# Optimization experiments

Measured on AMD Instinct MI355X. Metric: run time of the kernel, lower is better.

The kernel has to match this reference:

```python
import jax, jax.numpy as jnp
import numpy as np
import math

B, C, F, W, NH = 2, 8, 1024, 512, 8
HD = F // NH


def conv2d(x, w, b):
    # NCHW 3x3 same-padding conv with bias
    y = jax.lax.conv_general_dilated(x, w, (1, 1), [(1, 1), (1, 1)],
                                     dimension_numbers=('NCHW', 'OIHW', 'NCHW'))
    return y + b[None, :, None, None]


def mc_linear(x, w):
    # per-channel linear over the feature (h) axis: (b,c,h,w) x (c,f,h) -> (b,c,f,w)
    return jnp.einsum('bchw,cfh->bcfw', x, w)


def split_heads(t):
    # (b,c,f,w) -> transpose(2,3) -> (b,c,w,f) -> (b,c,w,nh,hd) -> (b,c,nh,w,hd)
    b, c, f, w = t.shape
    return jnp.transpose(t.transpose(0, 1, 3, 2).reshape(b, c, w, NH, HD), (0, 1, 3, 2, 4))


def rotate_queries_or_keys(x):
    # lucidrains-style interleaved rotary over the sequence axis (dim -2)
    d, w = x.shape[-1], x.shape[-2]
    inv_freq = 1.0 / (10000.0 ** (jnp.arange(0, d, 2, dtype=jnp.float32) / d))
    freqs = jnp.arange(w, dtype=jnp.float32)[:, None] * inv_freq[None, :]  # (w, d/2)
    freqs = jnp.repeat(freqs, 2, axis=-1)  # (w, d)
    cos, sin = jnp.cos(freqs), jnp.sin(freqs)
    xp = x.reshape(*x.shape[:-1], d // 2, 2)
    x1, x2 = xp[..., 0], xp[..., 1]
    x_rot = jnp.stack((-x2, x1), axis=-1).reshape(x.shape)
    return x * cos + x_rot * sin


def _forward(x, prev_qk, wq_conv, bq_conv, wq_lin, wk_conv, bk_conv, wk_lin,
             wv_conv, bv_conv, wv_lin, wo_lin):
    b, c, h, w = x.shape
    q = rotate_queries_or_keys(split_heads(mc_linear(conv2d(x, wq_conv, bq_conv), wq_lin)))
    k = rotate_queries_or_keys(split_heads(mc_linear(conv2d(x, wk_conv, bk_conv), wk_lin)))
    v = split_heads(mc_linear(conv2d(x, wv_conv, bv_conv), wv_lin))
    # NOTE: original scales by sqrt(h) == sqrt(features), not sqrt(head_dim)
    qk = jnp.einsum('bcnqd,bcnkd->bcnqk', q, k) / math.sqrt(h) + prev_qk
    a = jnp.einsum('bcnqk,bcnkd->bcnqd', jax.nn.softmax(qk, axis=-1), v)
    a = jnp.transpose(a, (0, 1, 3, 2, 4)).reshape(b, c, w, h).transpose(0, 1, 3, 2)
    out = mc_linear(a, wo_lin)
    return out, qk


def setup_inputs() -> dict:
    key = jax.random.key(0)
    ks = jax.random.split(key, 10)
    s = 0.02
    return {
        'x': jax.random.normal(ks[0], (B, C, F, W), dtype=jnp.float32),
        'prev_qk': jax.random.normal(ks[1], (B, C, NH, W, W), dtype=jnp.float32) * 0.1,
        'wq_conv': jax.random.normal(ks[2], (C, C, 3, 3), dtype=jnp.float32) * s,
        'bq_conv': jnp.zeros((C,), dtype=jnp.float32),
        'wq_lin': jax.random.normal(ks[3], (C, F, F), dtype=jnp.float32) * s,
        'wk_conv': jax.random.normal(ks[4], (C, C, 3, 3), dtype=jnp.float32) * s,
        'bk_conv': jnp.zeros((C,), dtype=jnp.float32),
        'wk_lin': jax.random.normal(ks[5], (C, F, F), dtype=jnp.float32) * s,
        'wv_conv': jax.random.normal(ks[6], (C, C, 3, 3), dtype=jnp.float32) * s,
        'bv_conv': jnp.zeros((C,), dtype=jnp.float32),
        'wv_lin': jax.random.normal(ks[7], (C, F, F), dtype=jnp.float32) * s,
        'wo_lin': jax.random.normal(ks[8], (C, F, F), dtype=jnp.float32) * s,
    }


def reference(x, prev_qk, wq_conv, bq_conv, wq_lin, wk_conv, bk_conv, wk_lin,
              wv_conv, bv_conv, wv_lin, wo_lin):
    return _forward(x, prev_qk, wq_conv, bq_conv, wq_lin, wk_conv, bk_conv, wk_lin,
                    wv_conv, bv_conv, wv_lin, wo_lin)
```

## Files before the change

kernel.cpp:

```cpp
#include <hip/hip_runtime.h>
#include <stdint.h>


typedef float f32x4 __attribute__((ext_vector_type(4)));
typedef short s16x8 __attribute__((ext_vector_type(8)));

__device__ __forceinline__ short f2bf(float f) {
  union { float f; uint32_t u; } v; v.f = f;
  uint32_t r = v.u + 0x7FFFu + ((v.u >> 16) & 1u);
  return (short)(r >> 16);
}

__device__ __forceinline__ void g2l16(const void* g, void* l) {
  __builtin_amdgcn_global_load_lds(
      (const __attribute__((address_space(1))) void*)g,
      (__attribute__((address_space(3))) void*)l, 16, 0, 0);
}

__device__ __forceinline__ void gemm_core(const short* __restrict__ A,
                                          const short* __restrict__ B,
                                          int K, short* sA, short* sB,
                                          f32x4 (*acc)[4]) {
  const int tid = threadIdx.x;
  const int lane = tid & 63;
  const int wv = tid >> 6;
  const int wm = wv >> 1, wn = wv & 1;
  const int q = lane >> 4, cix = lane & 15;

  for (int k0 = 0; k0 < K; k0 += 32) {
    __syncthreads();
#pragma unroll
    for (int i = 0; i < 2; ++i) {
      int seg = wv + 4 * i;
      int m = seg * 16 + (lane >> 2);
      int ko = (lane & 3) * 8;
      g2l16(B + (size_t)m * K + k0 + ko, sB + seg * 512);
    }
#pragma unroll
    for (int i = 0; i < 2; ++i) {
      int seg = wv + 4 * i;
      int m = seg * 16 + (lane >> 2);
      int ko = (lane & 3) * 8;
      g2l16(A + (size_t)m * K + k0 + ko, sA + seg * 512);
    }
    __syncthreads();
    s16x8 afr[4], bfr[4];
#pragma unroll
    for (int i = 0; i < 4; ++i)
      afr[i] = *(const s16x8*)(sA + (wm * 64 + i * 16 + cix) * 32 + q * 8);
#pragma unroll
    for (int i = 0; i < 4; ++i)
      bfr[i] = *(const s16x8*)(sB + (wn * 64 + i * 16 + cix) * 32 + q * 8);
#pragma unroll
    for (int i = 0; i < 4; ++i)
#pragma unroll
      for (int j = 0; j < 4; ++j)
        acc[i][j] = __builtin_amdgcn_mfma_f32_16x16x32_bf16(afr[i], bfr[j],
                                                            acc[i][j], 0, 0, 0);
  }
}

__global__ void __launch_bounds__(256) k_cvt(
    const float* __restrict__ w0, const float* __restrict__ w1,
    const float* __restrict__ w2, const float* __restrict__ w3,
    short* __restrict__ Wb) {
  size_t i = (size_t)blockIdx.x * 256 + threadIdx.x;
#pragma unroll
  for (int r = 0; r < 4; ++r) {
    const float* s = (r == 0) ? w0 : (r == 1) ? w1 : (r == 2) ? w2 : w3;
    size_t v = i + (size_t)r * 2097152;
    float4 f = *(const float4*)(s + (i << 2));
    short4 o;
    o.x = f2bf(f.x); o.y = f2bf(f.y); o.z = f2bf(f.z); o.w = f2bf(f.w);
    *(short4*)(Wb + (v << 2)) = o;
  }
}

__global__ void __launch_bounds__(256) k_conv(
    const float* __restrict__ x,
    const float* __restrict__ wqc, const float* __restrict__ bqc,
    const float* __restrict__ wkc, const float* __restrict__ bkc,
    const float* __restrict__ wvc, const float* __restrict__ bvc,
    short* __restrict__ Yt) {
  __shared__ float xs[8][66][19];
  const int h0 = blockIdx.x * 64, w0 = blockIdx.y * 16, b = blockIdx.z;
  const int tid = threadIdx.x;
  for (int idx = tid; idx < 8 * 66 * 18; idx += 256) {
    int c = idx / (66 * 18);
    int rem = idx % (66 * 18);
    int r = rem / 18, cc = rem % 18;
    int h = h0 + r - 1, w = w0 + cc - 1;
    float v = 0.f;
    if (h >= 0 && h < 1024 && w >= 0 && w < 512)
      v = x[(((size_t)b * 8 + c) << 10 | (unsigned)h) * 512 + w];
    xs[c][r][cc] = v;
  }
  __syncthreads();
  const int hh = tid & 63;
  const int wv4 = tid >> 6;
  const size_t hgl = h0 + hh;
  for (int proj = 0; proj < 3; ++proj) {
    const float* wc = (proj == 0) ? wqc : ((proj == 1) ? wkc : wvc);
    const float* bc = (proj == 0) ? bqc : ((proj == 1) ? bkc : bvc);
    float a[4][8];
#pragma unroll
    for (int jj = 0; jj < 4; ++jj)
#pragma unroll
      for (int co = 0; co < 8; ++co) a[jj][co] = bc[co];
    for (int ci = 0; ci < 8; ++ci)
#pragma unroll
      for (int dh = 0; dh < 3; ++dh)
#pragma unroll
        for (int dw = 0; dw < 3; ++dw) {
          float xv[4];
#pragma unroll
          for (int jj = 0; jj < 4; ++jj)
            xv[jj] = xs[ci][hh + dh][wv4 * 4 + jj + dw];
          const int wi = ci * 9 + dh * 3 + dw;
#pragma unroll
          for (int co = 0; co < 8; ++co) {
            float wgt = wc[co * 72 + wi];
#pragma unroll
            for (int jj = 0; jj < 4; ++jj) a[jj][co] = fmaf(xv[jj], wgt, a[jj][co]);
          }
        }
#pragma unroll
    for (int jj = 0; jj < 4; ++jj) {
      size_t col = (size_t)b * 512 + w0 + wv4 * 4 + jj;
#pragma unroll
      for (int co = 0; co < 8; ++co)
        Yt[((size_t)(proj * 8 + co) << 20) + (col << 10) + hgl] = f2bf(a[jj][co]);
    }
  }
}

__global__ void __launch_bounds__(256) k_qkv(
    const short* __restrict__ Wb, const short* __restrict__ Yt,
    short* __restrict__ Qr, short* __restrict__ Kr, short* __restrict__ Vt) {
  __shared__ short sA[128 * 32], sB[128 * 32];
  const int L = blockIdx.x;
  const int lin = (L & 7) * 192 + (L >> 3);
  const int g = lin >> 6;
  const int t = lin & 63;
  const int proj = g >> 3, cq = g & 7;
  const int mt = t >> 3, nt = t & 7;
  const short* A = Wb + ((size_t)g << 20) + ((size_t)mt << 17);
  const short* B = Yt + ((size_t)g << 20) + ((size_t)nt << 17);
  const f32x4 fzero = {0.f, 0.f, 0.f, 0.f};
  f32x4 acc[4][4];
#pragma unroll
  for (int i = 0; i < 4; ++i)
#pragma unroll
    for (int j = 0; j < 4; ++j) acc[i][j] = fzero;
  gemm_core(A, B, 1024, sA, sB, acc);

  const int lane = threadIdx.x & 63, wv = threadIdx.x >> 6;
  const int wm = wv >> 1, wn = wv & 1, q = lane >> 4, cix = lane & 15;
  const int head = mt;
  if (proj == 2) {
#pragma unroll
    for (int mi = 0; mi < 4; ++mi) {
      int rbase = wm * 64 + mi * 16 + q * 4;
#pragma unroll
      for (int ni = 0; ni < 4; ++ni) {
        int col = nt * 128 + wn * 64 + ni * 16 + cix;
        int b = col >> 9, wpos = col & 511;
        size_t base = ((size_t)((cq * 8 + head) * 2 + b) << 16) +
                      ((size_t)rbase << 9) + wpos;
        f32x4 v = acc[mi][ni];
        Vt[base] = f2bf(v[0]);
        Vt[base + 512] = f2bf(v[1]);
        Vt[base + 1024] = f2bf(v[2]);
        Vt[base + 1536] = f2bf(v[3]);
      }
    }
  } else {
    short* QKp = proj ? Kr : Qr;
#pragma unroll
    for (int mi = 0; mi < 4; ++mi) {
      int rbase = wm * 64 + mi * 16 + q * 4;
      int j0 = rbase >> 1;
      float if0 = exp2f(-0.20762050593046f * (float)j0);
      float if1 = exp2f(-0.20762050593046f * (float)(j0 + 1));
#pragma unroll
      for (int ni = 0; ni < 4; ++ni) {
        int col = nt * 128 + wn * 64 + ni * 16 + cix;
        int b = col >> 9, wpos = col & 511;
        float fw = (float)wpos;
        float s0, c0, s1, c1;
        __sincosf(fw * if0, &s0, &c0);
        __sincosf(fw * if1, &s1, &c1);
        f32x4 v = acc[mi][ni];
        short4 pk;
        pk.x = f2bf(v[0] * c0 - v[1] * s0);
        pk.y = f2bf(v[1] * c0 + v[0] * s0);
        pk.z = f2bf(v[2] * c1 - v[3] * s1);
        pk.w = f2bf(v[3] * c1 + v[2] * s1);
        *(short4*)&QKp[((size_t)(((cq * 8 + head) * 2 + b) * 512 + wpos) << 7) +
                       rbase] = pk;
      }
    }
  }
}

__global__ void __launch_bounds__(256) k_attn(
    const short* __restrict__ Qr, const short* __restrict__ Kr,
    const short* __restrict__ Vt, const float* __restrict__ prevqk,
    float* __restrict__ qk, short* __restrict__ At) {
  __shared__ short smem[128 * 136];
  __shared__ float psum[128][2];
  short* sA = smem;
  short* sB = smem + 128 * 32;
  short* Pt = smem;
  const int tid = threadIdx.x, lane = tid & 63, wv = tid >> 6;
  const int wm = wv >> 1, wn = wv & 1, q = lane >> 4, cix = lane & 15;
  const int qt = blockIdx.x, bcn = blockIdx.y;
  const int b = bcn >> 6, cch = (bcn >> 3) & 7, nh = bcn & 7;
  const size_t qrb = ((size_t)((cch * 8 + nh) * 2 + b)) << 16;
  const size_t rowg0 = (size_t)bcn * 512 + qt * 128;
  const short* A = Qr + qrb + ((size_t)qt << 14);

  const f32x4 fzero = {0.f, 0.f, 0.f, 0.f};
  f32x4 accO[4][4];
  float lsum[4][4];
#pragma unroll
  for (int i = 0; i < 4; ++i)
#pragma unroll
    for (int j = 0; j < 4; ++j) { accO[i][j] = fzero; lsum[i][j] = 0.f; }

  for (int kt = 0; kt < 4; ++kt) {
    f32x4 accS[4][4];
#pragma unroll
    for (int i = 0; i < 4; ++i)
#pragma unroll
      for (int j = 0; j < 4; ++j) accS[i][j] = fzero;
    gemm_core(A, Kr + qrb + ((size_t)kt << 14), 128, sA, sB, accS);

#pragma unroll
    for (int mi = 0; mi < 4; ++mi) {
#pragma unroll
      for (int ni = 0; ni < 4; ++ni) {
        int rl = wm * 64 + mi * 16 + q * 4;
        int cl = kt * 128 + wn * 64 + ni * 16 + cix;
        size_t base = ((rowg0 + rl) << 9) + cl;
#pragma unroll
        for (int r = 0; r < 4; ++r) {
          float s = accS[mi][ni][r] * 0.03125f + prevqk[base + (size_t)r * 512];
          qk[base + (size_t)r * 512] = s;
          accS[mi][ni][r] = s;
        }
      }
    }
    __syncthreads();
#pragma unroll
    for (int mi = 0; mi < 4; ++mi) {
#pragma unroll
      for (int r = 0; r < 4; ++r) {
        int row = wm * 64 + mi * 16 + q * 4 + r;
        float rs = 0.f;
#pragma unroll
        for (int ni = 0; ni < 4; ++ni) {
          float p = __expf(accS[mi][ni][r]);
          rs += p;
          Pt[row * 136 + wn * 64 + ni * 16 + cix] = f2bf(p);
        }
        lsum[mi][r] += rs;
      }
    }
    __syncthreads();
#pragma unroll
    for (int s4 = 0; s4 < 4; ++s4) {
      s16x8 afr[4], bfr[4];
#pragma unroll
      for (int i = 0; i < 4; ++i)
        afr[i] = *(const s16x8*)&Pt[(wm * 64 + i * 16 + cix) * 136 + s4 * 32 + q * 8];
#pragma unroll
      for (int i = 0; i < 4; ++i)
        bfr[i] = *(const s16x8*)&Vt[qrb + ((size_t)(wn * 64 + i * 16 + cix) << 9) +
                                    kt * 128 + s4 * 32 + q * 8];
#pragma unroll
      for (int i = 0; i < 4; ++i)
#pragma unroll
        for (int j = 0; j < 4; ++j)
          accO[i][j] = __builtin_amdgcn_mfma_f32_16x16x32_bf16(afr[i], bfr[j],
                                                               accO[i][j], 0, 0, 0);
    }
  }
#pragma unroll
  for (int mi = 0; mi < 4; ++mi)
#pragma unroll
    for (int r = 0; r < 4; ++r) {
      float se = lsum[mi][r];
      se += __shfl_xor(se, 1);
      se += __shfl_xor(se, 2);
      se += __shfl_xor(se, 4);
      se += __shfl_xor(se, 8);
      if (cix == 0) psum[wm * 64 + mi * 16 + q * 4 + r][wn] = se;
    }
  __syncthreads();
#pragma unroll
  for (int mi = 0; mi < 4; ++mi) {
    int rl = wm * 64 + mi * 16 + q * 4;
    float iL[4];
#pragma unroll
    for (int r = 0; r < 4; ++r)
      iL[r] = 1.0f / (psum[rl + r][0] + psum[rl + r][1]);
    int wq = qt * 128 + rl;
#pragma unroll
    for (int ni = 0; ni < 4; ++ni) {
      int dl = wn * 64 + ni * 16 + cix;
      size_t ob = (((size_t)cch << 10) + b * 512 + wq) * 1024 + nh * 128 + dl;
      f32x4 v = accO[mi][ni];
      At[ob] = f2bf(v[0] * iL[0]);
      At[ob + 1024] = f2bf(v[1] * iL[1]);
      At[ob + 2048] = f2bf(v[2] * iL[2]);
      At[ob + 3072] = f2bf(v[3] * iL[3]);
    }
  }
}

__global__ void __launch_bounds__(256) k_out(
    const short* __restrict__ At, const short* __restrict__ Wob,
    float* __restrict__ outp) {
  __shared__ short sA[128 * 32], sB[128 * 32];
  const int L = blockIdx.x;
  const int lin = (L & 7) * 64 + (L >> 3);
  const int c = lin >> 6;
  const int t = lin & 63;
  const int mt = t >> 3, nt = t & 7;
  const short* A = At + ((size_t)c << 20) + ((size_t)mt << 17);
  const short* B = Wob + ((size_t)c << 20) + ((size_t)nt << 17);
  const f32x4 fzero = {0.f, 0.f, 0.f, 0.f};
  f32x4 acc[4][4];
#pragma unroll
  for (int i = 0; i < 4; ++i)
#pragma unroll
    for (int j = 0; j < 4; ++j) acc[i][j] = fzero;
  gemm_core(A, B, 1024, sA, sB, acc);

  const int lane = threadIdx.x & 63, wv = threadIdx.x >> 6;
  const int wm = wv >> 1, wn = wv & 1, q = lane >> 4, cix = lane & 15;
#pragma unroll
  for (int mi = 0; mi < 4; ++mi) {
    int colm = mt * 128 + wm * 64 + mi * 16 + q * 4;
    int b = colm >> 9, w = colm & 511;
#pragma unroll
    for (int ni = 0; ni < 4; ++ni) {
      int f = nt * 128 + wn * 64 + ni * 16 + cix;
      f32x4 v = acc[mi][ni];
      float4 st; st.x = v[0]; st.y = v[1]; st.z = v[2]; st.w = v[3];
      *(float4*)&outp[((((size_t)b * 8 + c) << 10) + f) * 512 + w] = st;
    }
  }
}

extern "C" void kernel_launch(void* const* d_in, const int* in_sizes, int n_in,
                              void* d_out, int out_size, void* d_ws,
                              size_t ws_size, hipStream_t stream) {
  const float* x = (const float*)d_in[0];
  const float* prevqk = (const float*)d_in[1];
  const float* wqc = (const float*)d_in[2];
  const float* bqc = (const float*)d_in[3];
  const float* wql = (const float*)d_in[4];
  const float* wkc = (const float*)d_in[5];
  const float* bkc = (const float*)d_in[6];
  const float* wkl = (const float*)d_in[7];
  const float* wvc = (const float*)d_in[8];
  const float* bvc = (const float*)d_in[9];
  const float* wvl = (const float*)d_in[10];
  const float* wol = (const float*)d_in[11];
  float* outp = (float*)d_out;
  float* qk = outp + 8388608;

  char* ws = (char*)d_ws;
  short* Wb = (short*)ws;
  short* Yt = (short*)(ws + 67108864);
  short* Qr = (short*)(ws + 117440512);
  short* Kr = (short*)(ws + 134217728);
  short* Vt = (short*)(ws + 150994944);
  short* At = (short*)(ws + 67108864);
  short* Wob = Wb + ((size_t)24 << 20);

  k_cvt<<<dim3(8192), 256, 0, stream>>>(wql, wkl, wvl, wol, Wb);
  k_conv<<<dim3(16, 32, 2), 256, 0, stream>>>(x, wqc, bqc, wkc, bkc, wvc, bvc, Yt);
  k_qkv<<<dim3(1536), 256, 0, stream>>>(Wb, Yt, Qr, Kr, Vt);
  k_attn<<<dim3(4, 128), 256, 0, stream>>>(Qr, Kr, Vt, prevqk, qk, At);
  k_out<<<dim3(512), 256, 0, stream>>>(At, Wob, outp);
}
```

Baseline: 603.3 us.

## Keep Q tile resident in LDS and software-pipeline prev_qk loads in attention kernel

The attention kernel now loads the 128x128 Q tile into swizzled LDS once per block instead of restaging it with K through gemm_core on every key tile. K fragments are read straight from global memory into MFMA operands. The prev_qk loads are double-buffered in registers across row chunks so they overlap the scale/exp/store work, and the softmax-exp step is merged into the same pass, which removes one barrier. It adds launch_bounds(256,2), more LDS (separate Q and P buffers) and higher register pressure, which could reduce occupancy or cause spills.

```diff
diff --git a/kernel.cpp b/kernel.cpp
--- a/kernel.cpp
+++ b/kernel.cpp
@@ -203,22 +203,32 @@
   }
 }
 
-__global__ void __launch_bounds__(256) k_attn(
+__global__ void __launch_bounds__(256, 2) k_attn(
     const short* __restrict__ Qr, const short* __restrict__ Kr,
     const short* __restrict__ Vt, const float* __restrict__ prevqk,
     float* __restrict__ qk, short* __restrict__ At) {
-  __shared__ short smem[128 * 136];
+  __shared__ short Qs[128 * 128];
+  __shared__ short Pt[128 * 136];
   __shared__ float psum[128][2];
-  short* sA = smem;
-  short* sB = smem + 128 * 32;
-  short* Pt = smem;
   const int tid = threadIdx.x, lane = tid & 63, wv = tid >> 6;
   const int wm = wv >> 1, wn = wv & 1, q = lane >> 4, cix = lane & 15;
   const int qt = blockIdx.x, bcn = blockIdx.y;
   const int b = bcn >> 6, cch = (bcn >> 3) & 7, nh = bcn & 7;
   const size_t qrb = ((size_t)((cch * 8 + nh) * 2 + b)) << 16;
   const size_t rowg0 = (size_t)bcn * 512 + qt * 128;
-  const short* A = Qr + qrb + ((size_t)qt << 14);
+  const int arow = wm * 64;
+
+  {
+    const char* Qg = (const char*)(Qr + qrb + ((size_t)qt << 14));
+#pragma unroll
+    for (int i = 0; i < 8; ++i) {
+      int Lb = i * 4096 + wv * 1024;
+      int L = Lb + (lane << 4);
+      int src = (L & ~255) | ((L & 255) ^ (((L >> 8) & 15) << 4));
+      g2l16(Qg + src, (char*)Qs + Lb);
+    }
+  }
+  __syncthreads();
 
   const f32x4 fzero = {0.f, 0.f, 0.f, 0.f};
   f32x4 accO[4][4];
@@ -228,64 +238,104 @@
 #pragma unroll
     for (int j = 0; j < 4; ++j) { accO[i][j] = fzero; lsum[i][j] = 0.f; }
 
+  float pvA[16], pvB[16];
+
+#pragma unroll 1
   for (int kt = 0; kt < 4; ++kt) {
+    const int colb = kt * 128 + wn * 64 + cix;
     f32x4 accS[4][4];
 #pragma unroll
     for (int i = 0; i < 4; ++i)
 #pragma unroll
       for (int j = 0; j < 4; ++j) accS[i][j] = fzero;
-    gemm_core(A, Kr + qrb + ((size_t)kt << 14), 128, sA, sB, accS);
-
-#pragma unroll
-    for (int mi = 0; mi < 4; ++mi) {
-#pragma unroll
-      for (int ni = 0; ni < 4; ++ni) {
-        int rl = wm * 64 + mi * 16 + q * 4;
-        int cl = kt * 128 + wn * 64 + ni * 16 + cix;
-        size_t base = ((rowg0 + rl) << 9) + cl;
+
+#pragma unroll
+    for (int ni = 0; ni < 4; ++ni)
+#pragma unroll
+      for (int r = 0; r < 4; ++r)
+        pvA[ni * 4 + r] =
+            prevqk[((rowg0 + arow + q * 4 + r) << 9) + colb + ni * 16];
+
+    const short* Kbase = Kr + qrb + ((size_t)kt << 14);
+#pragma unroll
+    for (int kk = 0; kk < 4; ++kk) {
+      s16x8 afr[4], bfr[4];
+      const int cb = kk * 64 + q * 16;
+#pragma unroll
+      for (int ni = 0; ni < 4; ++ni)
+        bfr[ni] = *(const s16x8*)(Kbase +
+            ((size_t)(wn * 64 + ni * 16 + cix) << 7) + kk * 32 + q * 8);
+#pragma unroll
+      for (int mi = 0; mi < 4; ++mi) {
+        const int row = arow + mi * 16 + cix;
+        afr[mi] = *(const s16x8*)((const char*)Qs + row * 256 +
+                                  (cb ^ ((row & 15) << 4)));
+      }
+#pragma unroll
+      for (int mi = 0; mi < 4; ++mi)
+#pragma unroll
+        for (int ni = 0; ni < 4; ++ni)
+          accS[mi][ni] = __builtin_amdgcn_mfma_f32_16x16x32_bf16(
+              afr[mi], bfr[ni], accS[mi][ni], 0, 0, 0);
+    }
+
+    auto ldchunk = [&](int mi, float* dst) {
+#pragma unroll
+      for (int ni = 0; ni < 4; ++ni)
+#pragma unroll
+        for (int r = 0; r < 4; ++r)
+          dst[ni * 4 + r] =
+              prevqk[((rowg0 + arow + mi * 16 + q * 4 + r) << 9) +
+                     colb + ni * 16];
+    };
+    auto process = [&](int mi, const float* pv) {
+      float rs[4] = {0.f, 0.f, 0.f, 0.f};
+#pragma unroll
+      for (int ni = 0; ni < 4; ++ni)
 #pragma unroll
         for (int r = 0; r < 4; ++r) {
-          float s = accS[mi][ni][r] * 0.03125f + prevqk[base + (size_t)r * 512];
-          qk[base + (size_t)r * 512] = s;
-          accS[mi][ni][r] = s;
+          float s = accS[mi][ni][r] * 0.03125f + pv[ni * 4 + r];
+          qk[((rowg0 + arow + mi * 16 + q * 4 + r) << 9) + colb + ni * 16] = s;
+          float p = __expf(s);
+          rs[r] += p;
+          Pt[(arow + mi * 16 + q * 4 + r) * 136 + wn * 64 + ni * 16 + cix] =
+              f2bf(p);
         }
-      }
-    }
+#pragma unroll
+      for (int r = 0; r < 4; ++r) lsum[mi][r] += rs[r];
+    };
+    ldchunk(1, pvB);
+    process(0, pvA);
+    ldchunk(2, pvA);
+    process(1, pvB);
+    ldchunk(3, pvB);
+    process(2, pvA);
+    process(3, pvB);
+
     __syncthreads();
-#pragma unroll
-    for (int mi = 0; mi < 4; ++mi) {
-#pragma unroll
-      for (int r = 0; r < 4; ++r) {
-        int row = wm * 64 + mi * 16 + q * 4 + r;
-        float rs = 0.f;
-#pragma unroll
-        for (int ni = 0; ni < 4; ++ni) {
-          float p = __expf(accS[mi][ni][r]);
-          rs += p;
-          Pt[row * 136 + wn * 64 + ni * 16 + cix] = f2bf(p);
-        }
-        lsum[mi][r] += rs;
-      }
-    }
-    __syncthreads();
+
 #pragma unroll
     for (int s4 = 0; s4 < 4; ++s4) {
       s16x8 afr[4], bfr[4];
 #pragma unroll
       for (int i = 0; i < 4; ++i)
-        afr[i] = *(const s16x8*)&Pt[(wm * 64 + i * 16 + cix) * 136 + s4 * 32 + q * 8];
+        afr[i] =
+            *(const s16x8*)&Pt[(arow + i * 16 + cix) * 136 + s4 * 32 + q * 8];
 #pragma unroll
       for (int i = 0; i < 4; ++i)
-        bfr[i] = *(const s16x8*)&Vt[qrb + ((size_t)(wn * 64 + i * 16 + cix) << 9) +
+        bfr[i] = *(const s16x8*)&Vt[qrb +
+                                    ((size_t)(wn * 64 + i * 16 + cix) << 9) +
                                     kt * 128 + s4 * 32 + q * 8];
 #pragma unroll
       for (int i = 0; i < 4; ++i)
 #pragma unroll
         for (int j = 0; j < 4; ++j)
-          accO[i][j] = __builtin_amdgcn_mfma_f32_16x16x32_bf16(afr[i], bfr[j],
-                                                               accO[i][j], 0, 0, 0);
-    }
-  }
+          accO[i][j] = __builtin_amdgcn_mfma_f32_16x16x32_bf16(
+              afr[i], bfr[j], accO[i][j], 0, 0, 0);
+    }
+    __syncthreads();
+  }
+
 #pragma unroll
   for (int mi = 0; mi < 4; ++mi)
 #pragma unroll
@@ -295,12 +345,12 @@
       se += __shfl_xor(se, 2);
       se += __shfl_xor(se, 4);
       se += __shfl_xor(se, 8);
-      if (cix == 0) psum[wm * 64 + mi * 16 + q * 4 + r][wn] = se;
+      if (cix == 0) psum[arow + mi * 16 + q * 4 + r][wn] = se;
     }
   __syncthreads();
 #pragma unroll
   for (int mi = 0; mi < 4; ++mi) {
-    int rl = wm * 64 + mi * 16 + q * 4;
+    int rl = arow + mi * 16 + q * 4;
     float iL[4];
 #pragma unroll
     for (int r = 0; r < 4; ++r)
```

After: 581.9 us. -3.5%, faster.
